# Performance work log

Hardware: AMD Instinct MI355X
Metric: run time of the kernel (lower is better)

Reference implementation:

```python
import jax, jax.numpy as jnp
import numpy as np

EMBED = 1024
HEADS = 16
HEAD_DIM = EMBED // HEADS


def setup_inputs() -> dict:
    key = jax.random.key(0)
    ks = jax.random.split(key, 11)
    B, S = 4, 2048
    scale = 1.0 / np.sqrt(EMBED)
    inp = {
        "query": jax.random.normal(ks[0], (B, S, EMBED), dtype=jnp.float32),
        "key": jax.random.normal(ks[1], (B, S, EMBED), dtype=jnp.float32),
        "value": jax.random.normal(ks[2], (B, S, EMBED), dtype=jnp.float32),
        "Wq": jax.random.normal(ks[3], (EMBED, EMBED), dtype=jnp.float32) * scale,
        "bq": jnp.zeros((EMBED,), dtype=jnp.float32),
        "Wk": jax.random.normal(ks[4], (EMBED, EMBED), dtype=jnp.float32) * scale,
        "bk": jnp.zeros((EMBED,), dtype=jnp.float32),
        "Wv": jax.random.normal(ks[5], (EMBED, EMBED), dtype=jnp.float32) * scale,
        "bv": jnp.zeros((EMBED,), dtype=jnp.float32),
        "Wo": jax.random.normal(ks[6], (EMBED, EMBED), dtype=jnp.float32) * scale,
        "bo": jnp.zeros((EMBED,), dtype=jnp.float32),
    }
    return inp


def _split_heads(x):
    # [B,S,E] -> [B,H,S,D]
    B, S, _ = x.shape
    return x.reshape(B, S, HEADS, HEAD_DIM).transpose(0, 2, 1, 3)


def reference(query, key, value, Wq, bq, Wk, bk, Wv, bv, Wo, bo):
    B, S, _ = query.shape
    q = _split_heads(query @ Wq.T + bq)   # [B,H,S,D]
    k = _split_heads(key @ Wk.T + bk)
    v = _split_heads(value @ Wv.T + bv)
    scores = jnp.einsum("bhqd,bhkd->bhqk", q, k) / jnp.sqrt(jnp.float32(HEAD_DIM))
    attn = jax.nn.softmax(scores, axis=-1)
    out = jnp.einsum("bhqk,bhkd->bhqd", attn, v)  # [B,H,S,D]
    out = out.transpose(0, 2, 1, 3).reshape(B, S, EMBED)
    return out @ Wo.T + bo
```

## Files before the change

### kernel.cpp

```cpp
#include <hip/hip_runtime.h>

typedef _Float16 f16;
typedef __attribute__((ext_vector_type(2))) __fp16 fp16x2_raw;
typedef __attribute__((ext_vector_type(4))) _Float16 f16x4;
typedef __attribute__((ext_vector_type(8))) _Float16 f16x8;
typedef __attribute__((ext_vector_type(4))) float f32x4;
typedef __attribute__((ext_vector_type(16))) float f32x16;
typedef __attribute__((ext_vector_type(2))) unsigned int u32x2;

#define NB 4
#define NS 2048
#define NE 1024
#define NH 16
#define ND 64
#define NM (NB*NS)

__device__ __forceinline__ void gld16(const void* g, void* l) {
  __builtin_amdgcn_global_load_lds((const __attribute__((address_space(1))) unsigned int*)g,
                                   (__attribute__((address_space(3))) unsigned int*)l, 16, 0, 0);
}

__device__ __forceinline__ unsigned cvt2h(float a, float b) {
  fp16x2_raw r = __builtin_amdgcn_cvt_pkrtz(a, b);
  return __builtin_bit_cast(unsigned, r);
}

__device__ __forceinline__ void plswap(unsigned& a, unsigned& b) {
  asm volatile("v_permlane32_swap_b32 %0, %1" : "+v"(a), "+v"(b));
}

__global__ __launch_bounds__(256) void cvt_all(const float* __restrict__ s0, const float* __restrict__ s1,
                                               const float* __restrict__ s2, const float* __restrict__ s3,
                                               const float* __restrict__ s4, const float* __restrict__ s5,
                                               const float* __restrict__ s6, f16* __restrict__ dst) {
  const int X = NM*NE/4;
  const int W = NE*NE/4;
  const int total = 3*X + 4*W;
  int idx = blockIdx.x * blockDim.x + threadIdx.x;
  int stride = gridDim.x * blockDim.x;
  for (int i = idx; i < total; i += stride) {
    const float* src; int off;
    if      (i <   X)     { src = s0; off = i; }
    else if (i < 2*X)     { src = s1; off = i - X; }
    else if (i < 3*X)     { src = s2; off = i - 2*X; }
    else if (i < 3*X+W)   { src = s3; off = i - 3*X; }
    else if (i < 3*X+2*W) { src = s4; off = i - (3*X+W); }
    else if (i < 3*X+3*W) { src = s5; off = i - (3*X+2*W); }
    else                  { src = s6; off = i - (3*X+3*W); }
    float4 v = ((const float4*)src)[off];
    f16x4 o;
    o[0] = (_Float16)v.x; o[1] = (_Float16)v.y; o[2] = (_Float16)v.z; o[3] = (_Float16)v.w;
    ((f16x4*)dst)[i] = o;
  }
}

template<bool OUTF32>
__global__ __launch_bounds__(256)
void gemm_bt(const f16* __restrict__ A, const f16* __restrict__ Bw,
             const float* __restrict__ bias, float* __restrict__ Cf,
             f16* __restrict__ Ch, int M, int N, int K)
{
  __shared__ __align__(16) f16 As[128*32];
  __shared__ __align__(16) f16 Bs[128*32];
  const int t = threadIdx.x;
  const int l = t & 63, w = t >> 6;
  const int wr = w >> 1, wc = w & 1;
  const int m0 = blockIdx.y * 128, n0 = blockIdx.x * 128;

  f32x4 acc[4][4];
  #pragma unroll
  for (int i = 0; i < 4; ++i)
    #pragma unroll
    for (int j = 0; j < 4; ++j)
      acc[i][j] = f32x4{0.f, 0.f, 0.f, 0.f};

  const int off0 = (w*2+0)*1024 + l*16;
  const int off1 = (w*2+1)*1024 + l*16;
  const int row0 = off0 >> 6, k0 = (off0 & 63) >> 1;
  const int row1 = off1 >> 6, k1 = (off1 & 63) >> 1;
  const f16* a0 = A  + (size_t)(m0+row0)*K + k0;
  const f16* a1 = A  + (size_t)(m0+row1)*K + k1;
  const f16* b0 = Bw + (size_t)(n0+row0)*K + k0;
  const f16* b1 = Bw + (size_t)(n0+row1)*K + k1;
  f16* As0 = As + off0/2; f16* As1 = As + off1/2;
  f16* Bs0 = Bs + off0/2; f16* Bs1 = Bs + off1/2;

  const int aoff = (wr*64 + (l&15))*32 + ((l>>4)<<3);
  const int boff = (wc*64 + (l&15))*32 + ((l>>4)<<3);

  for (int kt = 0; kt < K; kt += 32) {
    __syncthreads();
    gld16(a0 + kt, As0);
    gld16(a1 + kt, As1);
    gld16(b0 + kt, Bs0);
    gld16(b1 + kt, Bs1);
    __syncthreads();
    f16x8 af[4], bf[4];
    #pragma unroll
    for (int i = 0; i < 4; ++i) af[i] = *(const f16x8*)(As + aoff + i*512);
    #pragma unroll
    for (int j = 0; j < 4; ++j) bf[j] = *(const f16x8*)(Bs + boff + j*512);
    #pragma unroll
    for (int i = 0; i < 4; ++i)
      #pragma unroll
      for (int j = 0; j < 4; ++j)
        acc[i][j] = __builtin_amdgcn_mfma_f32_16x16x32_f16(af[i], bf[j], acc[i][j], 0, 0, 0);
  }

  #pragma unroll
  for (int j = 0; j < 4; ++j) {
    const int col = n0 + wc*64 + j*16 + (l & 15);
    const float bb = bias[col];
    #pragma unroll
    for (int i = 0; i < 4; ++i) {
      const int rowb = m0 + wr*64 + i*16 + ((l>>4)<<2);
      #pragma unroll
      for (int r = 0; r < 4; ++r) {
        float v = acc[i][j][r] + bb;
        if constexpr (OUTF32) Cf[(size_t)(rowb+r)*N + col] = v;
        else                  Ch[(size_t)(rowb+r)*N + col] = (f16)v;
      }
    }
  }
}

__global__ __launch_bounds__(256, 4)
void attn_kernel(const f16* __restrict__ Q, const f16* __restrict__ K,
                 const f16* __restrict__ V, f16* __restrict__ O)
{
  __shared__ __align__(16) f16 S_lds[8192];

  const int t = threadIdx.x, l = t & 63, w = t >> 6;
  const int lq = l & 31, hi = l >> 5;

  const int lin = blockIdx.x + (blockIdx.y << 4);
  const int xcd = lin & 7, jj = lin >> 3;
  const int bh = xcd * 8 + (jj >> 4);
  const int qt = jj & 15;
  const int b = bh >> 4, h = bh & 15;
  const size_t base = (size_t)b * NS * NE + (size_t)h * ND;
  const int q = qt*128 + w*32 + lq;

  f16x8 bq[4];
  #pragma unroll
  for (int ks = 0; ks < 4; ++ks)
    bq[ks] = *(const f16x8*)&Q[base + (size_t)q*NE + ks*16 + hi*8];
  asm volatile("s_waitcnt vmcnt(0)" ::: "memory");

  f32x16 o[2];
  #pragma unroll
  for (int dt = 0; dt < 2; ++dt)
    #pragma unroll
    for (int r = 0; r < 16; ++r) o[dt][r] = 0.f;
  float m2 = -3e38f, lsum = 0.f;
  const float K2 = 0.125f * 1.44269504089f;

  const int krow0 = w*16 + (l>>3);
  const int kgran = ((l&7) ^ (l>>3)) * 8;
  const f16* kSrc0 = K + base + (size_t)krow0*NE + kgran;
  const f16* kSrc1 = kSrc0 + (size_t)8*NE;
  f16* kDst0 = &S_lds[0] + (w*2+0)*512 + l*8;
  f16* kDst1 = &S_lds[0] + (w*2+1)*512 + l*8;

  const f16* vSrc = V + base + (size_t)l*NE + w*16;
  const char* ksb = (const char*)&S_lds[0];
  char* vtb = (char*)&S_lds[4096];

  const size_t tileAdv = (size_t)64 * NE;

  for (int it = 0; it < 32; ++it) {
    const size_t g = (size_t)it * tileAdv;
    __syncthreads();
    gld16(kSrc0 + g, kDst0);
    gld16(kSrc1 + g, kDst1);
    {
      f16x8 va = *(const f16x8*)(vSrc + g);
      f16x8 vb = *(const f16x8*)(vSrc + g + 8);
      #pragma unroll
      for (int i = 0; i < 8; ++i) {
        const int d0 = w*16 + i, d1 = w*16 + 8 + i;
        *(f16*)(vtb + ((d0*128 + l*2) ^ ((i & 7) << 4))) = va[i];
        *(f16*)(vtb + ((d1*128 + l*2) ^ ((i & 7) << 4))) = vb[i];
      }
    }
    __syncthreads();

    f32x16 s[2];
    #pragma unroll
    for (int ct = 0; ct < 2; ++ct)
      #pragma unroll
      for (int r = 0; r < 16; ++r) s[ct][r] = 0.f;
    __builtin_amdgcn_s_setprio(1);
    #pragma unroll
    for (int ct = 0; ct < 2; ++ct) {
      const int krow = ct*32 + lq;
      const int rswz = (krow & 7) << 4;
      #pragma unroll
      for (int ks = 0; ks < 4; ++ks) {
        f16x8 ak = *(const f16x8*)(ksb + ((krow*128 + ks*32 + hi*16) ^ rswz));
        s[ct] = __builtin_amdgcn_mfma_f32_32x32x16_f16(ak, bq[ks], s[ct], 0, 0, 0);
      }
    }
    __builtin_amdgcn_s_setprio(0);

    float mx = fmaxf(s[0][0], s[1][0]);
    #pragma unroll
    for (int r = 1; r < 16; ++r) mx = fmaxf(mx, fmaxf(s[0][r], s[1][r]));
    mx *= K2;
    mx = fmaxf(mx, __shfl_xor(mx, 32));
    const float mnew = fmaxf(m2, mx);
    const float alpha = __builtin_amdgcn_exp2f(m2 - mnew);
    m2 = mnew;
    float ps = 0.f;
    #pragma unroll
    for (int ct = 0; ct < 2; ++ct)
      #pragma unroll
      for (int r = 0; r < 16; ++r) {
        float p = __builtin_amdgcn_exp2f(s[ct][r]*K2 - m2);
        s[ct][r] = p;
        ps += p;
      }
    lsum = lsum*alpha + ps;
    #pragma unroll
    for (int dt = 0; dt < 2; ++dt)
      #pragma unroll
      for (int r = 0; r < 16; ++r) o[dt][r] *= alpha;

    f16x8 pa[4];
    #pragma unroll
    for (int ct = 0; ct < 2; ++ct) {
      unsigned wd[8];
      #pragma unroll
      for (int m = 0; m < 4; ++m)
        #pragma unroll
        for (int hh = 0; hh < 2; ++hh)
          wd[m*2 + hh] = cvt2h(s[ct][4*m + 2*hh], s[ct][4*m + 2*hh + 1]);
      #pragma unroll
      for (int ks2 = 0; ks2 < 2; ++ks2) {
        unsigned a0 = wd[(2*ks2)*2 + 0], b0 = wd[(2*ks2+1)*2 + 0];
        unsigned a1 = wd[(2*ks2)*2 + 1], b1 = wd[(2*ks2+1)*2 + 1];
        plswap(a0, b0);
        plswap(a1, b1);
        union { unsigned u[4]; f16x8 v; } pp;
        pp.u[0] = a0; pp.u[1] = a1; pp.u[2] = b0; pp.u[3] = b1;
        pa[ct*2 + ks2] = pp.v;
      }
    }

    __builtin_amdgcn_s_setprio(1);
    #pragma unroll
    for (int ks = 0; ks < 4; ++ks)
      #pragma unroll
      for (int dt = 0; dt < 2; ++dt) {
        const int drow = dt*32 + lq;
        f16x8 av = *(const f16x8*)(vtb + ((drow*128 + ks*32 + hi*16) ^ ((drow & 7) << 4)));
        o[dt] = __builtin_amdgcn_mfma_f32_32x32x16_f16(av, pa[ks], o[dt], 0, 0, 0);
      }
    __builtin_amdgcn_s_setprio(0);
  }

  const float lt = lsum + __shfl_xor(lsum, 32);
  const float linv = 1.0f / lt;
  #pragma unroll
  for (int dt = 0; dt < 2; ++dt)
    #pragma unroll
    for (int m = 0; m < 4; ++m) {
      u32x2 st;
      st.x = cvt2h(o[dt][4*m+0]*linv, o[dt][4*m+1]*linv);
      st.y = cvt2h(o[dt][4*m+2]*linv, o[dt][4*m+3]*linv);
      const int d = dt*32 + 8*m + 4*hi;
      *(u32x2*)&O[base + (size_t)q*NE + d] = st;
    }
}

extern "C" void kernel_launch(void* const* d_in, const int* in_sizes, int n_in,
                              void* d_out, int out_size, void* d_ws, size_t ws_size,
                              hipStream_t stream)
{
  const float* q_in = (const float*)d_in[0];
  const float* k_in = (const float*)d_in[1];
  const float* v_in = (const float*)d_in[2];
  const float* Wq = (const float*)d_in[3];
  const float* bq = (const float*)d_in[4];
  const float* Wk = (const float*)d_in[5];
  const float* bk = (const float*)d_in[6];
  const float* Wv = (const float*)d_in[7];
  const float* bv = (const float*)d_in[8];
  const float* Wo = (const float*)d_in[9];
  const float* bo = (const float*)d_in[10];

  char* ws = (char*)d_ws;
  f16* Xq   = (f16*)(ws + 0);
  f16* Xk   = (f16*)(ws + 16777216);
  f16* Xv   = (f16*)(ws + 33554432);
  f16* Wq16 = (f16*)(ws + 50331648);
  f16* Wk16 = (f16*)(ws + 52428800);
  f16* Wv16 = (f16*)(ws + 54525952);
  f16* Wo16 = (f16*)(ws + 56623104);
  f16* Qp   = (f16*)(ws + 58720256);
  f16* Kp   = (f16*)(ws + 75497472);
  f16* Vp   = (f16*)(ws + 92274688);
  f16* Op   = (f16*)(ws + 109051904);

  cvt_all<<<2048, 256, 0, stream>>>(q_in, k_in, v_in, Wq, Wk, Wv, Wo, Xq);

  dim3 gg(8, 64);
  gemm_bt<false><<<gg, 256, 0, stream>>>(Xq, Wq16, bq, nullptr, Qp, NM, NE, NE);
  gemm_bt<false><<<gg, 256, 0, stream>>>(Xk, Wk16, bk, nullptr, Kp, NM, NE, NE);
  gemm_bt<false><<<gg, 256, 0, stream>>>(Xv, Wv16, bv, nullptr, Vp, NM, NE, NE);

  attn_kernel<<<dim3(16, 64), 256, 0, stream>>>(Qp, Kp, Vp, Op);

  gemm_bt<true><<<gg, 256, 0, stream>>>(Op, Wo16, bo, (float*)d_out, nullptr, NM, NE, NE);
}
```

Measured before the change: 266.1 us.

## Double-buffer K/V tiles in attention kernel to overlap loads with MFMA

Doubles the LDS buffer in the attention kernel and prefetches the next K/V tile (async global-to-LDS for K, register load for V) while the current tile is being computed. It also drops one of the two per-iteration barriers. The aim is to hide global memory latency behind the QK and PV matrix work. In exchange, LDS use per block doubles to 32KB, which may lower occupancy under launch_bounds(256,4), and the extra V registers add pressure.

Result: no change. 263.8 us (-0.9%).

```diff
diff --git a/kernel.cpp b/kernel.cpp
--- a/kernel.cpp
+++ b/kernel.cpp
@@ -128,7 +128,7 @@
 void attn_kernel(const f16* __restrict__ Q, const f16* __restrict__ K,
                  const f16* __restrict__ V, f16* __restrict__ O)
 {
-  __shared__ __align__(16) f16 S_lds[8192];
+  __shared__ __align__(16) f16 S_lds[16384];
 
   const int t = threadIdx.x, l = t & 63, w = t >> 6;
   const int lq = l & 31, hi = l >> 5;
@@ -159,31 +159,41 @@
   const int kgran = ((l&7) ^ (l>>3)) * 8;
   const f16* kSrc0 = K + base + (size_t)krow0*NE + kgran;
   const f16* kSrc1 = kSrc0 + (size_t)8*NE;
-  f16* kDst0 = &S_lds[0] + (w*2+0)*512 + l*8;
-  f16* kDst1 = &S_lds[0] + (w*2+1)*512 + l*8;
-
   const f16* vSrc = V + base + (size_t)l*NE + w*16;
-  const char* ksb = (const char*)&S_lds[0];
-  char* vtb = (char*)&S_lds[4096];
 
   const size_t tileAdv = (size_t)64 * NE;
+  const int kd0 = (w*2+0)*512 + l*8;
+  const int kd1 = (w*2+1)*512 + l*8;
+
+  f16x8 va, vb;
+  {
+    gld16(kSrc0, &S_lds[0] + kd0);
+    gld16(kSrc1, &S_lds[0] + kd1);
+    va = *(const f16x8*)(vSrc);
+    vb = *(const f16x8*)(vSrc + 8);
+    asm volatile("s_waitcnt vmcnt(0)" ::: "memory");
+    char* vt0 = (char*)&S_lds[4096];
+    #pragma unroll
+    for (int i = 0; i < 8; ++i) {
+      const int d0 = w*16 + i, d1 = w*16 + 8 + i;
+      *(f16*)(vt0 + ((d0*128 + l*2) ^ ((i & 7) << 4))) = va[i];
+      *(f16*)(vt0 + ((d1*128 + l*2) ^ ((i & 7) << 4))) = vb[i];
+    }
+  }
+  __syncthreads();
 
   for (int it = 0; it < 32; ++it) {
-    const size_t g = (size_t)it * tileAdv;
-    __syncthreads();
-    gld16(kSrc0 + g, kDst0);
-    gld16(kSrc1 + g, kDst1);
-    {
-      f16x8 va = *(const f16x8*)(vSrc + g);
-      f16x8 vb = *(const f16x8*)(vSrc + g + 8);
-      #pragma unroll
-      for (int i = 0; i < 8; ++i) {
-        const int d0 = w*16 + i, d1 = w*16 + 8 + i;
-        *(f16*)(vtb + ((d0*128 + l*2) ^ ((i & 7) << 4))) = va[i];
-        *(f16*)(vtb + ((d1*128 + l*2) ^ ((i & 7) << 4))) = vb[i];
-      }
-    }
-    __syncthreads();
+    const int cur = it & 1, nb = cur ^ 1;
+    const char* ksb = (const char*)(&S_lds[cur*8192]);
+    const char* vtb = (const char*)(&S_lds[cur*8192 + 4096]);
+
+    if (it < 31) {
+      const size_t g = (size_t)(it+1) * tileAdv;
+      gld16(kSrc0 + g, &S_lds[nb*8192] + kd0);
+      gld16(kSrc1 + g, &S_lds[nb*8192] + kd1);
+      va = *(const f16x8*)(vSrc + g);
+      vb = *(const f16x8*)(vSrc + g + 8);
+    }
 
     f32x16 s[2];
     #pragma unroll
@@ -257,6 +267,18 @@
         o[dt] = __builtin_amdgcn_mfma_f32_32x32x16_f16(av, pa[ks], o[dt], 0, 0, 0);
       }
     __builtin_amdgcn_s_setprio(0);
+
+    if (it < 31) {
+      asm volatile("s_waitcnt vmcnt(0)" ::: "memory");
+      char* vtn = (char*)(&S_lds[nb*8192 + 4096]);
+      #pragma unroll
+      for (int i = 0; i < 8; ++i) {
+        const int d0 = w*16 + i, d1 = w*16 + 8 + i;
+        *(f16*)(vtn + ((d0*128 + l*2) ^ ((i & 7) << 4))) = va[i];
+        *(f16*)(vtn + ((d1*128 + l*2) ^ ((i & 7) << 4))) = vb[i];
+      }
+      __syncthreads();
+    }
   }
 
   const float lt = lsum + __shfl_xor(lsum, 32);
```
